# Performance work log

Measured on AMD Instinct MI355X. Metric: run time of the kernel, lower is better.

Reference implementation:

```python
import jax, jax.numpy as jnp
import numpy as np

EPS = 1e-5  # torch LayerNorm default
H = 8       # heads_num


def _ln(t, g, b):
    m = jnp.mean(t, axis=-1, keepdims=True)
    v = jnp.var(t, axis=-1, keepdims=True)
    return (t - m) / jnp.sqrt(v + EPS) * g + b


def setup_inputs() -> dict:
    key = jax.random.key(0)
    ks = jax.random.split(key, 12)
    B, S, Dq, Dk, Dff = 4, 2048, 512, 768, 2048
    def w(k, shape, scale=0.02):
        return jax.random.normal(k, shape, jnp.float32) * scale
    return {
        "x": jax.random.normal(ks[0], (B, S, Dq), jnp.float32),
        "y": jax.random.normal(ks[1], (B, S, Dk), jnp.float32),
        # cross-attention projections (stored [in, out]; linear_q/k/v have no bias)
        "Wq": w(ks[2], (Dq, Dq)), "Wk": w(ks[3], (Dk, Dq)), "Wv": w(ks[4], (Dk, Dq)),
        "Wo": w(ks[5], (Dq, Dq)), "bo": jnp.zeros((Dq,), jnp.float32),
        # nn.MultiheadAttention packed in-projection and out-projection
        "mha_w_in": w(ks[6], (Dq, 3 * Dq)), "mha_b_in": jnp.zeros((3 * Dq,), jnp.float32),
        "mha_wo": w(ks[7], (Dq, Dq)), "mha_bo": jnp.zeros((Dq,), jnp.float32),
        # 4 LayerNorms
        "ln1_g": jnp.ones((Dq,), jnp.float32), "ln1_b": jnp.zeros((Dq,), jnp.float32),
        "ln2_g": jnp.ones((Dk,), jnp.float32), "ln2_b": jnp.zeros((Dk,), jnp.float32),
        "ln3_g": jnp.ones((Dq,), jnp.float32), "ln3_b": jnp.zeros((Dq,), jnp.float32),
        "ln4_g": jnp.ones((Dq,), jnp.float32), "ln4_b": jnp.zeros((Dq,), jnp.float32),
        # dense MLP (moe=False branch)
        "mlp_w1": w(ks[8], (Dq, Dff)), "mlp_b1": jnp.zeros((Dff,), jnp.float32),
        "mlp_w2": w(ks[9], (Dff, Dq)), "mlp_b2": jnp.zeros((Dq,), jnp.float32),
    }


def reference(x, y, Wq, Wk, Wv, Wo, bo, mha_w_in, mha_b_in, mha_wo, mha_bo,
              ln1_g, ln1_b, ln2_g, ln2_b, ln3_g, ln3_b, ln4_g, ln4_b,
              mlp_w1, mlp_b1, mlp_w2, mlp_b2):
    B, S, D = x.shape
    hd = D // H
    inv_sqrt_hd = 1.0 / np.sqrt(hd).astype(np.float32)

    xn = _ln(x, ln1_g, ln1_b)
    yn = _ln(y, ln2_g, ln2_b)

    # ---- Multi_CrossAttention: manual QK^T softmax V over true seq axis ----
    q = (xn @ Wq).reshape(B, S, H, hd)
    k = (yn @ Wk).reshape(B, -1, H, hd)
    v = (yn @ Wv).reshape(B, -1, H, hd)
    scores = jnp.einsum('bqhd,bkhd->bhqk', q, k) * inv_sqrt_hd  # [B,H,S,S] (512 MB)
    attn = jax.nn.softmax(scores, axis=-1)
    ctx = jnp.einsum('bhqk,bkhd->bqhd', attn, v).reshape(B, S, D)
    ca = ctx @ Wo + bo

    h = _ln(ca + xn, ln3_g, ln3_b)

    # ---- nn.MultiheadAttention (batch_first=False!): axis 0 is the sequence ----
    qkv = h @ mha_w_in + mha_b_in  # [L=B, N=S, 3D]
    q2, k2, v2 = jnp.split(qkv, 3, axis=-1)
    L, N = q2.shape[0], q2.shape[1]
    q2 = q2.reshape(L, N, H, hd)
    k2 = k2.reshape(L, N, H, hd)
    v2 = v2.reshape(L, N, H, hd)
    s2 = jnp.einsum('lnhd,mnhd->nhlm', q2, k2) * inv_sqrt_hd  # [N,H,L,L]
    a2 = jax.nn.softmax(s2, axis=-1)
    sa = jnp.einsum('nhlm,mnhd->lnhd', a2, v2).reshape(L, N, D) @ mha_wo + mha_bo

    h2 = _ln(sa + h, ln4_g, ln4_b)

    # ---- dense MLP (GELU exact, dropout=0) ----
    mlp = jax.nn.gelu(h2 @ mlp_w1 + mlp_b1, approximate=False) @ mlp_w2 + mlp_b2
    return mlp + h2
```

## Files before the change

kernel.cpp:

```cpp
#include <hip/hip_runtime.h>
#include <math.h>

typedef unsigned short u16;
typedef __attribute__((ext_vector_type(8))) short bf8;
typedef __attribute__((ext_vector_type(4))) float f4;
typedef __attribute__((ext_vector_type(16))) float f32x16;
typedef __attribute__((ext_vector_type(4))) unsigned int u32x4;
typedef __attribute__((ext_vector_type(2))) unsigned int u32x2;
typedef __attribute__((ext_vector_type(4))) unsigned short u16x4;
typedef __attribute__((ext_vector_type(8))) unsigned short u16x8;

__device__ __forceinline__ float bf2f(u16 a){
  unsigned u = ((unsigned)a) << 16;
  float f; __builtin_memcpy(&f, &u, 4);
  return f;
}
__device__ __forceinline__ u16 f2bf(float f){
  unsigned u; __builtin_memcpy(&u, &f, 4);
  u += 0x7fffu + ((u >> 16) & 1u);
  return (u16)(u >> 16);
}
__device__ __forceinline__ unsigned cvtpk(float a, float b){
  unsigned r;
  asm("v_cvt_pk_bf16_f32 %0, %1, %2" : "=v"(r) : "v"(a), "v"(b));
  return r;
}
__device__ __forceinline__ void plswap(unsigned &a, unsigned &b){
  asm("v_permlane32_swap_b32 %0, %1" : "+v"(a), "+v"(b));
}
__device__ __forceinline__ void gload16(const u16* g, u16* l){
  __builtin_amdgcn_global_load_lds((const __attribute__((address_space(1))) void*)g,
                                   (__attribute__((address_space(3))) void*)l, 16, 0, 0);
}
__device__ __forceinline__ int xcd_swizzle(int orig, int nwg){
  const int qq = nwg >> 3, rr = nwg & 7;
  const int xcd = orig & 7, loc = orig >> 3;
  return (xcd < rr ? xcd * (qq + 1) : rr * (qq + 1) + (xcd - rr) * qq) + loc;
}
__device__ __forceinline__ float gelu_f(float v){
  const float vc = fminf(v, 10.f);
  const float z  = vc * (1.f + 0.044715f * vc * vc);
  const float e  = __builtin_amdgcn_exp2f(2.302208499f * z);
  return v * e * __builtin_amdgcn_rcpf(e + 1.f);
}

__global__ void k_transpose_all(
    const float* __restrict__ Wq, const float* __restrict__ Wk,
    const float* __restrict__ Wv, const float* __restrict__ Wo,
    const float* __restrict__ Win, const float* __restrict__ Wmo,
    const float* __restrict__ W1, const float* __restrict__ W2,
    u16* __restrict__ WqT, u16* __restrict__ WkT, u16* __restrict__ WvT,
    u16* __restrict__ WoT, u16* __restrict__ WinT, u16* __restrict__ WmoT,
    u16* __restrict__ W1T, u16* __restrict__ W2T)
{
  __shared__ float tile[32][33];
  const int tid = blockIdx.x;
  const float* in; u16* out; int R, C, lo;
  if (tid < 1280){
    if (tid < 256)       { in = Wq;  out = WqT;  R = 512; C = 512;  lo = 0; }
    else if (tid < 640)  { in = Wk;  out = WkT;  R = 768; C = 512;  lo = 256; }
    else if (tid < 1024) { in = Wv;  out = WvT;  R = 768; C = 512;  lo = 640; }
    else                 { in = Wo;  out = WoT;  R = 512; C = 512;  lo = 1024; }
  } else {
    if (tid < 2048)      { in = Win; out = WinT; R = 512; C = 1536; lo = 1280; }
    else if (tid < 2304) { in = Wmo; out = WmoT; R = 512; C = 512;  lo = 2048; }
    else if (tid < 3328) { in = W1;  out = W1T;  R = 512; C = 2048; lo = 2304; }
    else                 { in = W2;  out = W2T;  R = 2048; C = 512; lo = 3328; }
  }
  const int local = tid - lo;
  const int tpx = C >> 5;
  const int bx = (local % tpx) * 32, by = (local / tpx) * 32;
  const int tx = threadIdx.x, ty = threadIdx.y;
#pragma unroll
  for (int i = 0; i < 4; i++)
    tile[ty + i*8][tx] = in[(size_t)(by + ty + i*8) * C + bx + tx];
  __syncthreads();
#pragma unroll
  for (int i = 0; i < 4; i++)
    out[(size_t)(bx + ty + i*8) * R + by + tx] = f2bf(tile[tx][ty + i*8]);
}

__device__ __forceinline__ void ln_row_f32(
    const float* __restrict__ r, const float* __restrict__ gam,
    const float* __restrict__ bet, u16* __restrict__ outb, int D, int t)
{
  const int nv = D >> 8;
  float v[3] = {0.f, 0.f, 0.f};
  float s = 0.f, s2 = 0.f;
#pragma unroll
  for (int i = 0; i < 3; i++){
    if (i < nv){ float xx = r[t + i*256]; v[i] = xx; s += xx; s2 += xx*xx; }
  }
#pragma unroll
  for (int m = 32; m; m >>= 1){ s += __shfl_xor(s, m); s2 += __shfl_xor(s2, m); }
  __shared__ float rs[4], rq[4];
  const int wave = t >> 6;
  if ((t & 63) == 0){ rs[wave] = s; rq[wave] = s2; }
  __syncthreads();
  s  = rs[0] + rs[1] + rs[2] + rs[3];
  s2 = rq[0] + rq[1] + rq[2] + rq[3];
  const float mean = s / (float)D;
  const float var  = s2 / (float)D - mean * mean;
  const float rstd = rsqrtf(var + 1e-5f);
#pragma unroll
  for (int i = 0; i < 3; i++){
    if (i < nv){
      const int c = t + i*256;
      outb[c] = f2bf((v[i] - mean) * rstd * gam[c] + bet[c]);
    }
  }
}

__global__ __launch_bounds__(256) void k_layernorm12(
    const float* __restrict__ x, const float* __restrict__ y,
    const float* __restrict__ g1, const float* __restrict__ b1,
    const float* __restrict__ g2, const float* __restrict__ b2,
    u16* __restrict__ xnB, u16* __restrict__ ynB)
{
  const int row = blockIdx.x;
  if (row < 8192){
    ln_row_f32(x + (size_t)row * 512, g1, b1, xnB + (size_t)row * 512, 512, threadIdx.x);
  } else {
    const int r2 = row - 8192;
    ln_row_f32(y + (size_t)r2 * 768, g2, b2, ynB + (size_t)r2 * 768, 768, threadIdx.x);
  }
}

__global__ __launch_bounds__(256) void k_layernorm_b(
    const u16* __restrict__ in, const float* __restrict__ gam,
    const float* __restrict__ bet, u16* __restrict__ outb)
{
  const int row = blockIdx.x, t = threadIdx.x;
  const u16* r = in + (size_t)row * 512;
  const float v0 = bf2f(r[t]);
  const float v1 = bf2f(r[t + 256]);
  float s = v0 + v1, s2 = v0*v0 + v1*v1;
#pragma unroll
  for (int m = 32; m; m >>= 1){ s += __shfl_xor(s, m); s2 += __shfl_xor(s2, m); }
  __shared__ float rs[4], rq[4];
  const int wave = t >> 6;
  if ((t & 63) == 0){ rs[wave] = s; rq[wave] = s2; }
  __syncthreads();
  s  = rs[0] + rs[1] + rs[2] + rs[3];
  s2 = rq[0] + rq[1] + rq[2] + rq[3];
  const float mean = s * (1.f / 512.f);
  const float var  = s2 * (1.f / 512.f) - mean * mean;
  const float rstd = rsqrtf(var + 1e-5f);
  u16* o = outb + (size_t)row * 512;
  o[t]       = f2bf((v0 - mean) * rstd * gam[t] + bet[t]);
  o[t + 256] = f2bf((v1 - mean) * rstd * gam[t + 256] + bet[t + 256]);
}

template<int TM, int TN, bool BIAS, bool RES, bool GELU_ACT, int OUTM, bool QSC = false>
__global__ __launch_bounds__(256, 4) void k_gemm(
    const u16* __restrict__ A, const u16* __restrict__ BT,
    const float* __restrict__ bias, const u16* __restrict__ res,
    float* __restrict__ outf, u16* __restrict__ outb, u16* __restrict__ outb2,
    int M, int N, int K)
{
  constexpr int MF = TM / 32;
  constexpr int NF = TN / 32;
  constexpr int WM = TM / 2;
  constexpr int WN = TN / 2;
  __shared__ u16 Sb[(TM + TN) * 64];
  const int t = threadIdx.x;
  const int gx = gridDim.x;
  const int swz = xcd_swizzle(blockIdx.y * gx + blockIdx.x, gx * gridDim.y);
  const int m0 = (swz / gx) * TM, n0 = (swz % gx) * TN;
  const int wave = t >> 6, lane = t & 63;
  const int wm = wave >> 1, wn = wave & 1;
  const int l15 = lane & 15, lg = lane >> 4;
  const u16* Ag = A + (size_t)m0 * K;
  const u16* Bg = BT + (size_t)n0 * K;

  const int lrow = lane >> 3;
  const int csrc = (((lane & 7) ^ lrow) << 3);
  const u16* Agl = Ag + (size_t)lrow * K + csrc;
  const u16* Bgl = Bg + (size_t)lrow * K + csrc;

  f4 acc[MF][NF];
#pragma unroll
  for (int i = 0; i < MF; i++)
#pragma unroll
    for (int j = 0; j < NF; j++) acc[i][j] = (f4){0.f, 0.f, 0.f, 0.f};

  const int nK = K >> 6;
#pragma unroll
  for (int i = 0; i < TM/32; i++){
    const int rb = (i*4 + wave) * 8;
    gload16(Agl + (size_t)rb * K, &Sb[rb * 64]);
  }
#pragma unroll
  for (int i = 0; i < TN/32; i++){
    const int rb = (i*4 + wave) * 8;
    gload16(Bgl + (size_t)rb * K, &Sb[(TM + rb) * 64]);
  }
  asm volatile("s_waitcnt vmcnt(0)" ::: "memory");
  __syncthreads();

  for (int kt = 0;; kt++){
    const char* As = (const char*)&Sb[0];
    const char* Bs = (const char*)&Sb[TM * 64];
#pragma unroll
    for (int kc = 0; kc < 2; kc++){
      bf8 af[MF], bfr[NF];
      const int kb = kc*64 + lg*16;
#pragma unroll
      for (int mf = 0; mf < MF; mf++){
        const int row = wm*WM + mf*16 + l15;
        af[mf] = *(const bf8*)(As + row*128 + (kb ^ ((row & 7) << 4)));
      }
#pragma unroll
      for (int nf = 0; nf < NF; nf++){
        const int row = wn*WN + nf*16 + l15;
        bfr[nf] = *(const bf8*)(Bs + row*128 + (kb ^ ((row & 7) << 4)));
      }
#pragma unroll
      for (int mf = 0; mf < MF; mf++)
#pragma unroll
        for (int nf = 0; nf < NF; nf++)
          acc[mf][nf] = __builtin_amdgcn_mfma_f32_16x16x32_bf16(af[mf], bfr[nf], acc[mf][nf], 0, 0, 0);
    }
    if (kt + 1 == nK) break;
    __syncthreads();
    const int ko = (kt + 1) << 6;
#pragma unroll
    for (int i = 0; i < TM/32; i++){
      const int rb = (i*4 + wave) * 8;
      gload16(Agl + (size_t)rb * K + ko, &Sb[rb * 64]);
    }
#pragma unroll
    for (int i = 0; i < TN/32; i++){
      const int rb = (i*4 + wave) * 8;
      gload16(Bgl + (size_t)rb * K + ko, &Sb[(TM + rb) * 64]);
    }
    asm volatile("s_waitcnt vmcnt(0)" ::: "memory");
    __syncthreads();
  }
#pragma unroll
  for (int mf = 0; mf < MF; mf++){
#pragma unroll
    for (int nf = 0; nf < NF; nf++){
      const int colg = n0 + wn*WN + nf*16 + l15;
      const int rowg = m0 + wm*WM + mf*16 + lg*4;
      const float bv = BIAS ? bias[colg] : 0.f;
      float vv[4];
#pragma unroll
      for (int j = 0; j < 4; j++){
        float v = acc[mf][nf][j] + bv;
        if (RES) v += bf2f(res[(size_t)(rowg + j) * N + colg]);
        if (GELU_ACT) v = gelu_f(v);
        if (QSC) v *= 0.1803368801f;
        vv[j] = v;
      }
      if (OUTM == 0){
#pragma unroll
        for (int j = 0; j < 4; j++) outf[(size_t)(rowg + j) * N + colg] = vv[j];
      } else if (OUTM == 1){
#pragma unroll
        for (int j = 0; j < 4; j++) outb[(size_t)(rowg + j) * N + colg] = f2bf(vv[j]);
      } else if (OUTM == 2){
        const int bb = rowg >> 11, ss = rowg & 2047;
        u16x4 pk;
#pragma unroll
        for (int j = 0; j < 4; j++) pk[j] = f2bf(vv[j]);
        *(u16x4*)(outb + ((size_t)(bb*512 + colg)) * 2048 + ss) = pk;
      } else {
        if (n0 < 512){
#pragma unroll
          for (int j = 0; j < 4; j++) outb[(size_t)(rowg + j) * 512 + colg] = f2bf(vv[j]);
        } else {
          const int bb = rowg >> 11, ss = rowg & 2047;
          u16x4 pk;
#pragma unroll
          for (int j = 0; j < 4; j++) pk[j] = f2bf(vv[j]);
          *(u16x4*)(outb2 + ((size_t)(bb*512 + (colg - 512))) * 2048 + ss) = pk;
        }
      }
    }
  }
}

__global__ __launch_bounds__(256, 3) void k_flash(
    const u16* __restrict__ q, const u16* __restrict__ k,
    const u16* __restrict__ vt, u16* __restrict__ ctx)
{
  __shared__ u16 Kb[128 * 64];
  __shared__ u16 Vb[2][64 * 128];
  const int t = threadIdx.x;
  const int wave = t >> 6, lane = t & 63;
  const int l31 = lane & 31, hi = lane >> 5;
  const int id = blockIdx.y * 16 + blockIdx.x;
  const int swz = xcd_swizzle(id, 512);
  const int qb = swz & 15, bh = swz >> 4;
  const int b = bh >> 3, h = bh & 7;
  const int qrow0 = qb*128 + wave*32;

  bf8 qf[4];
  {
    const u16* qp = q + ((size_t)(b*2048 + qrow0 + l31)) * 512 + h*64 + hi*8;
    qf[0] = *(const bf8*)qp;
    qf[1] = *(const bf8*)(qp + 16);
    qf[2] = *(const bf8*)(qp + 32);
    qf[3] = *(const bf8*)(qp + 48);
  }

  const int lrow8 = lane >> 3;
  const int csK = (((lane & 7) ^ lrow8) << 3);
  const u16* kgl = k + ((size_t)(b*2048 + lrow8)) * 512 + h*64 + csK;
  const int lrow4 = lane >> 4;
  const int csVe = (((lane & 15) ^ lrow4) << 3);
  const int csVo = (((lane & 15) ^ (4 + lrow4)) << 3);
  const u16* vrow = vt + ((size_t)(b*512 + h*64 + lrow4)) * 2048;

  f32x16 o0, o1;
#pragma unroll
  for (int r = 0; r < 16; r++){ o0[r] = 0.f; o1[r] = 0.f; }
  float rl = 0.f;

#pragma unroll
  for (int i = 0; i < 4; i++){
    const int rb = (i*4 + wave) * 8;
    gload16(kgl + (size_t)rb * 512, &Kb[rb * 64]);
    const int sl = i*4 + wave;
    gload16(vrow + (size_t)(sl*4) * 2048 + ((sl & 1) ? csVo : csVe), &Vb[0][sl * 512]);
  }

  int cur = 0;
  for (int it = 0; it < 16; it++){
    asm volatile("s_waitcnt vmcnt(0)" ::: "memory");
    __syncthreads();
    if (it + 1 < 16){
      const int kt = (it + 1) << 7;
#pragma unroll
      for (int i = 0; i < 4; i++){
        const int sl = i*4 + wave;
        gload16(vrow + (size_t)(sl*4) * 2048 + kt + ((sl & 1) ? csVo : csVe),
                &Vb[cur^1][sl * 512]);
      }
    }
    const char* kbuf = (const char*)Kb;
    const char* vbuf = (const char*)Vb[cur];
    f32x16 s0, s1, s2, s3;
#pragma unroll
    for (int r = 0; r < 16; r++){ s0[r] = 0.f; s1[r] = 0.f; s2[r] = 0.f; s3[r] = 0.f; }
    __builtin_amdgcn_s_setprio(1);
#pragma unroll
    for (int ds = 0; ds < 4; ds++){
      const int off = ds*32 + hi*16;
      const int r0 = l31, r1 = 32 + l31, r2 = 64 + l31, r3 = 96 + l31;
      const bf8 k0 = *(const bf8*)(kbuf + r0*128 + (off ^ ((r0 & 7) << 4)));
      const bf8 k1 = *(const bf8*)(kbuf + r1*128 + (off ^ ((r1 & 7) << 4)));
      const bf8 k2 = *(const bf8*)(kbuf + r2*128 + (off ^ ((r2 & 7) << 4)));
      const bf8 k3 = *(const bf8*)(kbuf + r3*128 + (off ^ ((r3 & 7) << 4)));
      s0 = __builtin_amdgcn_mfma_f32_32x32x16_bf16(k0, qf[ds], s0, 0, 0, 0);
      s1 = __builtin_amdgcn_mfma_f32_32x32x16_bf16(k1, qf[ds], s1, 0, 0, 0);
      s2 = __builtin_amdgcn_mfma_f32_32x32x16_bf16(k2, qf[ds], s2, 0, 0, 0);
      s3 = __builtin_amdgcn_mfma_f32_32x32x16_bf16(k3, qf[ds], s3, 0, 0, 0);
    }
    __builtin_amdgcn_s_setprio(0);
    __syncthreads();
    if (it + 1 < 16){
      const int kt = (it + 1) << 7;
#pragma unroll
      for (int i = 0; i < 4; i++){
        const int rb = (i*4 + wave) * 8;
        gload16(kgl + (size_t)(kt + rb) * 512, &Kb[rb * 64]);
      }
    }
    float rsum = 0.f;
#define SMPV(SV, SUB)                                                          \
    {                                                                          \
      float pp[16];                                                            \
      _Pragma("unroll")                                                        \
      for (int r = 0; r < 16; r++) pp[r] = __builtin_amdgcn_exp2f(SV[r]);      \
      _Pragma("unroll")                                                        \
      for (int r = 0; r < 16; r++) rsum += pp[r];                              \
      unsigned w0 = cvtpk(pp[0],  pp[1]),  w1 = cvtpk(pp[2],  pp[3]);          \
      unsigned w2 = cvtpk(pp[4],  pp[5]),  w3 = cvtpk(pp[6],  pp[7]);          \
      unsigned w4 = cvtpk(pp[8],  pp[9]),  w5 = cvtpk(pp[10], pp[11]);         \
      unsigned w6 = cvtpk(pp[12], pp[13]), w7 = cvtpk(pp[14], pp[15]);         \
      plswap(w0, w2); plswap(w1, w3);                                          \
      plswap(w4, w6); plswap(w5, w7);                                          \
      u32x4 t0 = {w0, w1, w2, w3};                                             \
      u32x4 t1 = {w4, w5, w6, w7};                                             \
      bf8 pa0, pa1;                                                            \
      __builtin_memcpy(&pa0, &t0, 16);                                         \
      __builtin_memcpy(&pa1, &t1, 16);                                         \
      const int off0 = SUB*64 + hi*16;                                         \
      const int off1 = SUB*64 + 32 + hi*16;                                    \
      const int r0 = l31, r1 = 32 + l31;                                       \
      const bf8 va0 = *(const bf8*)(vbuf + r0*256 + (off0 ^ ((r0 & 7) << 4))); \
      const bf8 va1 = *(const bf8*)(vbuf + r1*256 + (off0 ^ ((r1 & 7) << 4))); \
      const bf8 vb0 = *(const bf8*)(vbuf + r0*256 + (off1 ^ ((r0 & 7) << 4))); \
      const bf8 vb1 = *(const bf8*)(vbuf + r1*256 + (off1 ^ ((r1 & 7) << 4))); \
      o0 = __builtin_amdgcn_mfma_f32_32x32x16_bf16(pa0, va0, o0, 0, 0, 0);     \
      o1 = __builtin_amdgcn_mfma_f32_32x32x16_bf16(pa0, va1, o1, 0, 0, 0);     \
      o0 = __builtin_amdgcn_mfma_f32_32x32x16_bf16(pa1, vb0, o0, 0, 0, 0);     \
      o1 = __builtin_amdgcn_mfma_f32_32x32x16_bf16(pa1, vb1, o1, 0, 0, 0);     \
    }
    SMPV(s0, 0)
    SMPV(s1, 1)
    SMPV(s2, 2)
    SMPV(s3, 3)
#undef SMPV
    rsum += __shfl_xor(rsum, 32);
    rl += rsum;
    cur ^= 1;
  }
  const float linv = 1.f / rl;
#pragma unroll
  for (int r = 0; r < 16; r++){
    const int crow = (r & 3) + 8*(r >> 2) + 4*hi;
    const float iv = __shfl(linv, crow);
    u16* cp = ctx + ((size_t)(b*2048 + qrow0 + crow)) * 512 + h*64 + l31;
    cp[0]  = f2bf(o0[r] * iv);
    cp[32] = f2bf(o1[r] * iv);
  }
}

__global__ __launch_bounds__(256) void k_mha_small(const u16* __restrict__ qkv,
                                                   u16* __restrict__ outb)
{
  const int tid = blockIdx.x * 256 + threadIdx.x;
  const int n = tid & 2047;
  const int hl = tid >> 11;
  const int h = hl >> 2, l = hl & 3;
  const u16* qp = qkv + ((size_t)l * 2048 + n) * 1536 + h*64;
  float qv[64];
#pragma unroll
  for (int i = 0; i < 8; i++){
    const bf8 c = *(const bf8*)(qp + i*8);
#pragma unroll
    for (int j2 = 0; j2 < 8; j2++) qv[i*8 + j2] = bf2f((u16)c[j2]) * 0.125f;
  }
  float sc[4];
#pragma unroll
  for (int m = 0; m < 4; m++){
    const u16* kp = qkv + ((size_t)m * 2048 + n) * 1536 + 512 + h*64;
    float a = 0.f;
#pragma unroll
    for (int i = 0; i < 8; i++){
      const bf8 c = *(const bf8*)(kp + i*8);
#pragma unroll
      for (int j2 = 0; j2 < 8; j2++) a += qv[i*8 + j2] * bf2f((u16)c[j2]);
    }
    sc[m] = a;
  }
  const float mx = fmaxf(fmaxf(sc[0], sc[1]), fmaxf(sc[2], sc[3]));
  float p[4]; float sum = 0.f;
#pragma unroll
  for (int m = 0; m < 4; m++){ p[m] = __expf(sc[m] - mx); sum += p[m]; }
  const float inv = 1.f / sum;
  float ov[64];
#pragma unroll
  for (int i = 0; i < 64; i++) ov[i] = 0.f;
#pragma unroll
  for (int m = 0; m < 4; m++){
    const float pw = p[m] * inv;
    const u16* vp = qkv + ((size_t)m * 2048 + n) * 1536 + 1024 + h*64;
#pragma unroll
    for (int i = 0; i < 8; i++){
      const bf8 c = *(const bf8*)(vp + i*8);
#pragma unroll
      for (int j2 = 0; j2 < 8; j2++) ov[i*8 + j2] += pw * bf2f((u16)c[j2]);
    }
  }
  u16* op = outb + ((size_t)l * 2048 + n) * 512 + h*64;
#pragma unroll
  for (int i = 0; i < 8; i++){
    u16x8 pk;
#pragma unroll
    for (int j2 = 0; j2 < 8; j2++) pk[j2] = f2bf(ov[i*8 + j2]);
    *(u16x8*)(op + i*8) = pk;
  }
}

extern "C" void kernel_launch(void* const* d_in, const int* in_sizes, int n_in,
                              void* d_out, int out_size, void* d_ws, size_t ws_size,
                              hipStream_t stream)
{
  (void)in_sizes; (void)n_in; (void)out_size; (void)ws_size;
  const float* x    = (const float*)d_in[0];
  const float* y    = (const float*)d_in[1];
  const float* Wq   = (const float*)d_in[2];
  const float* Wk   = (const float*)d_in[3];
  const float* Wv   = (const float*)d_in[4];
  const float* Wo   = (const float*)d_in[5];
  const float* bo   = (const float*)d_in[6];
  const float* Win  = (const float*)d_in[7];
  const float* bin  = (const float*)d_in[8];
  const float* Wmo  = (const float*)d_in[9];
  const float* bmo  = (const float*)d_in[10];
  const float* ln1g = (const float*)d_in[11];
  const float* ln1b = (const float*)d_in[12];
  const float* ln2g = (const float*)d_in[13];
  const float* ln2b = (const float*)d_in[14];
  const float* ln3g = (const float*)d_in[15];
  const float* ln3b = (const float*)d_in[16];
  const float* ln4g = (const float*)d_in[17];
  const float* ln4b = (const float*)d_in[18];
  const float* W1   = (const float*)d_in[19];
  const float* b1   = (const float*)d_in[20];
  const float* W2   = (const float*)d_in[21];
  const float* b2   = (const float*)d_in[22];

  char* ws = (char*)d_ws;
  const size_t MB = 1024 * 1024;
  u16* WqT  = (u16*)ws;
  u16* WkT  = WqT  + 512 * 512;
  u16* WvT  = WkT  + 512 * 768;
  u16* WoT  = WvT  + 512 * 768;
  u16* WinT = WoT  + 512 * 512;
  u16* WmoT = WinT + 1536 * 512;
  u16* W1T  = WmoT + 512 * 512;
  u16* W2T  = W1T  + 2048 * 512;
  u16* xnB  = (u16*)(ws +   9 * MB);
  u16* ynB  = (u16*)(ws +  17 * MB);
  u16* qB   = (u16*)(ws +  29 * MB);
  u16* kB   = (u16*)(ws +  37 * MB);
  u16* vtB  = (u16*)(ws +  45 * MB);
  u16* ctxB = (u16*)(ws +  53 * MB);
  u16* carB = (u16*)(ws +  61 * MB);
  u16* hB   = (u16*)(ws +  69 * MB);
  u16* qkvB = (u16*)(ws +  77 * MB);
  u16* saB  = (u16*)(ws + 101 * MB);
  u16* sarB = qB;
  u16* h2B  = kB;
  u16* t1B  = vtB;

  k_transpose_all<<<4352, dim3(32, 8), 0, stream>>>(
      Wq, Wk, Wv, Wo, Win, Wmo, W1, W2,
      WqT, WkT, WvT, WoT, WinT, WmoT, W1T, W2T);

  k_layernorm12<<<16384, 256, 0, stream>>>(x, y, ln1g, ln1b, ln2g, ln2b, xnB, ynB);

  k_gemm<64,128,false,false,false,1,true><<<dim3(4, 128), 256, 0, stream>>>(xnB, WqT, nullptr, nullptr, nullptr, qB, nullptr, 8192, 512, 512);
  k_gemm<64,128,false,false,false,3><<<dim3(8, 128), 256, 0, stream>>>(ynB, WkT, nullptr, nullptr, nullptr, kB, vtB,   8192, 1024, 768);

  k_flash<<<dim3(16, 32), 256, 0, stream>>>(qB, kB, vtB, ctxB);

  k_gemm<64,128,true,true,false,1><<<dim3(4, 128), 256, 0, stream>>>(ctxB, WoT, bo, xnB, nullptr, carB, nullptr, 8192, 512, 512);
  k_layernorm_b<<<8192, 256, 0, stream>>>(carB, ln3g, ln3b, hB);

  k_gemm<128,128,true,false,false,1><<<dim3(12, 64), 256, 0, stream>>>(hB, WinT, bin, nullptr, nullptr, qkvB, nullptr, 8192, 1536, 512);
  k_mha_small<<<256, 256, 0, stream>>>(qkvB, saB);
  k_gemm<64,128,true,true,false,1><<<dim3(4, 128), 256, 0, stream>>>(saB, WmoT, bmo, hB, nullptr, sarB, nullptr, 8192, 512, 512);
  k_layernorm_b<<<8192, 256, 0, stream>>>(sarB, ln4g, ln4b, h2B);

  k_gemm<128,128,true,false,true,1><<<dim3(16, 64), 256, 0, stream>>>(h2B, W1T, b1, nullptr, nullptr, t1B, nullptr, 8192, 2048, 512);
  k_gemm<64,128,true,true,false,0><<<dim3(4, 128), 256, 0, stream>>>(t1B, W2T, b2, h2B, (float*)d_out, nullptr, nullptr, 8192, 512, 2048);
}
```

Baseline: 212.0 us.

## Add 256x256-tile 512-thread GEMM kernel for QKV in-projection and MLP up-projection

```diff
diff --git a/kernel.cpp b/kernel.cpp
--- a/kernel.cpp
+++ b/kernel.cpp
@@ -276,6 +276,97 @@
           for (int j = 0; j < 4; j++) pk[j] = f2bf(vv[j]);
           *(u16x4*)(outb2 + ((size_t)(bb*512 + (colg - 512))) * 2048 + ss) = pk;
         }
+      }
+    }
+  }
+}
+
+template<bool BIAS, bool GELU_ACT>
+__global__ __launch_bounds__(512, 2) void k_gemm256(
+    const u16* __restrict__ A, const u16* __restrict__ BT,
+    const float* __restrict__ bias, u16* __restrict__ outb,
+    int M, int N, int K)
+{
+  __shared__ u16 Sb[2][512 * 64];
+  const int t = threadIdx.x;
+  const int gx = gridDim.x;
+  const int swz = xcd_swizzle(blockIdx.y * gx + blockIdx.x, gx * gridDim.y);
+  const int m0 = (swz / gx) * 256, n0 = (swz % gx) * 256;
+  const int wave = t >> 6, lane = t & 63;
+  const int wm = wave >> 2, wn = wave & 3;
+  const int l15 = lane & 15, lg = lane >> 4;
+  const u16* Ag = A + (size_t)m0 * K;
+  const u16* Bg = BT + (size_t)n0 * K;
+
+  const int lrow = lane >> 3;
+  const int csrc = (((lane & 7) ^ lrow) << 3);
+  const u16* Agl = Ag + (size_t)lrow * K + csrc;
+  const u16* Bgl = Bg + (size_t)lrow * K + csrc;
+
+  f4 acc[8][4];
+#pragma unroll
+  for (int i = 0; i < 8; i++)
+#pragma unroll
+    for (int j = 0; j < 4; j++) acc[i][j] = (f4){0.f, 0.f, 0.f, 0.f};
+
+  const int nK = K >> 6;
+  auto stage = [&](int kt, int bi){
+    u16* dst = &Sb[bi][0];
+    const int ko = kt << 6;
+#pragma unroll
+    for (int i = 0; i < 4; i++){
+      const int rb = (i*8 + wave) * 8;
+      gload16(Agl + (size_t)rb * K + ko, dst + rb * 64);
+      gload16(Bgl + (size_t)rb * K + ko, dst + (256 + rb) * 64);
+    }
+  };
+
+  stage(0, 0);
+  asm volatile("s_waitcnt vmcnt(0)" ::: "memory");
+  __syncthreads();
+
+  int cur = 0;
+  for (int kt = 0;; kt++){
+    if (kt + 1 < nK) stage(kt + 1, cur ^ 1);
+    const char* As = (const char*)&Sb[cur][0];
+    const char* Bs = (const char*)&Sb[cur][256 * 64];
+#pragma unroll
+    for (int kc = 0; kc < 2; kc++){
+      bf8 af[8], bfr[4];
+      const int kb = kc*64 + lg*16;
+#pragma unroll
+      for (int mf = 0; mf < 8; mf++){
+        const int row = wm*128 + mf*16 + l15;
+        af[mf] = *(const bf8*)(As + row*128 + (kb ^ ((row & 7) << 4)));
+      }
+#pragma unroll
+      for (int nf = 0; nf < 4; nf++){
+        const int row = wn*64 + nf*16 + l15;
+        bfr[nf] = *(const bf8*)(Bs + row*128 + (kb ^ ((row & 7) << 4)));
+      }
+#pragma unroll
+      for (int mf = 0; mf < 8; mf++)
+#pragma unroll
+        for (int nf = 0; nf < 4; nf++)
+          acc[mf][nf] = __builtin_amdgcn_mfma_f32_16x16x32_bf16(af[mf], bfr[nf], acc[mf][nf], 0, 0, 0);
+    }
+    if (kt + 1 == nK) break;
+    asm volatile("s_waitcnt vmcnt(0)" ::: "memory");
+    __syncthreads();
+    cur ^= 1;
+  }
+#pragma unroll
+  for (int mf = 0; mf < 8; mf++){
+#pragma unroll
+    for (int nf = 0; nf < 4; nf++){
+      const int colg = n0 + wn*64 + nf*16 + l15;
+      const int rowg = m0 + wm*128 + mf*16 + lg*4;
+      const float bv = BIAS ? bias[colg] : 0.f;
+#pragma unroll
+      for (int j = 0; j < 4; j++){
+        float v = acc[mf][nf][j] + bv;
+        if (GELU_ACT) v = gelu_f(v);
+        outb[(size_t)(rowg + j) * N + colg] = f2bf(v);
       }
     }
   }
@@ -543,11 +634,11 @@
   k_gemm<64,128,true,true,false,1><<<dim3(4, 128), 256, 0, stream>>>(ctxB, WoT, bo, xnB, nullptr, carB, nullptr, 8192, 512, 512);
   k_layernorm_b<<<8192, 256, 0, stream>>>(carB, ln3g, ln3b, hB);
 
-  k_gemm<128,128,true,false,false,1><<<dim3(12, 64), 256, 0, stream>>>(hB, WinT, bin, nullptr, nullptr, qkvB, nullptr, 8192, 1536, 512);
+  k_gemm256<true,false><<<dim3(6, 32), 512, 0, stream>>>(hB, WinT, bin, qkvB, 8192, 1536, 512);
   k_mha_small<<<256, 256, 0, stream>>>(qkvB, saB);
   k_gemm<64,128,true,true,false,1><<<dim3(4, 128), 256, 0, stream>>>(saB, WmoT, bmo, hB, nullptr, sarB, nullptr, 8192, 512, 512);
   k_layernorm_b<<<8192, 256, 0, stream>>>(sarB, ln4g, ln4b, h2B);
 
-  k_gemm<128,128,true,false,true,1><<<dim3(16, 64), 256, 0, stream>>>(h2B, W1T, b1, nullptr, nullptr, t1B, nullptr, 8192, 2048, 512);
+  k_gemm256<true,true><<<dim3(8, 32), 512, 0, stream>>>(h2B, W1T, b1, t1B, 8192, 2048, 512);
   k_gemm<64,128,true,true,false,0><<<dim3(4, 128), 256, 0, stream>>>(t1B, W2T, b2, h2B, (float*)d_out, nullptr, nullptr, 8192, 512, 2048);
 }
```

Result: no change. 215.6 us (+1.7%).
